# Optimization experiments

Hardware: AMD Instinct MI355X
Metric: run time of the kernel (lower is better)

## Reference

```python
import math
import jax, jax.numpy as jnp
import numpy as np

DIMS = 20
MULT = 8
K = (DIMS + 1) * MULT  # 168 mixture components
N = 524288
EPS = 1.0              # log_density default eps
BASE_COV = 0.1
LOG_NORM = -DIMS / 2 * math.log(2 * math.pi)


def setup_inputs() -> dict:
    key = jax.random.key(0)
    k1, k2, k3 = jax.random.split(key, 3)
    sample = jax.random.normal(k1, (N, DIMS), dtype=jnp.float32) * 0.3
    alpha = jax.random.normal(k2, (K,), dtype=jnp.float32) * 0.1
    mu = jax.random.uniform(k3, (K, DIMS), dtype=jnp.float32, minval=-0.5, maxval=0.5)
    cov = jnp.full((K, DIMS), BASE_COV, dtype=jnp.float32)
    return {"sample": sample, "alpha": alpha, "mu": mu, "cov": cov}


def reference(sample, alpha, mu, cov):
    # Faithful vectorization of the per-component Python loop in log_density.
    var = EPS ** 2
    weights = jax.nn.softmax(alpha)                       # [K]
    i = jnp.arange(K) // MULT                             # component group index, 0..DIMS
    d = jnp.arange(DIMS)
    # cov[:i] *= var  ->  scale first i dims of each component's cov by var
    scale = jnp.where(d[None, :] < i[:, None], var, 1.0)  # [K, D]
    inv = 1.0 / (cov * scale)                             # [K, D]
    # det_cov = var**i * (1/10)**(dims - i)  (exactly as in the source)
    fi = i.astype(jnp.float32)
    det_cov = var ** fi * BASE_COV ** (DIMS - fi)         # [K]
    sig_term = det_cov ** -0.5                            # [K]
    # quad[n,k] = sum_d (x[n,d]-mu[k,d])^2 * inv[k,d], expanded into GEMMs
    quad = (sample ** 2) @ inv.T \
           - 2.0 * (sample @ (mu * inv).T) \
           + jnp.sum(mu * mu * inv, axis=1)[None, :]      # [N, K]
    results = sig_term * jnp.exp(-0.5 * quad) * weights   # [N, K]
    density = results.sum(axis=1, keepdims=True)          # [N, 1]
    return jnp.log(density) + LOG_NORM
```

## Files before the change

kernel.cpp:

```cpp
#include <hip/hip_runtime.h>
#include <math.h>


#define DIMS     20
#define MULT     8
#define K_COMP   168
#define KC_PAD   176
#define BROW     72
#define BASE_COV 0.1f
#define LOG2E    1.4426950408889634f
#define LN2      0.6931471805599453f
#define LOG_NORM -18.378770664093453f
#define CPW      8
#define NB       1024

typedef _Float16 f16x8 __attribute__((ext_vector_type(8)));
typedef _Float16 f16x2 __attribute__((ext_vector_type(2)));
typedef float    f32x4 __attribute__((ext_vector_type(4)));
typedef unsigned int uint;
typedef uint u32x4 __attribute__((ext_vector_type(4)));

__device__ __forceinline__ uint pk(float lo, float hi) {
    return __builtin_bit_cast(uint, __builtin_amdgcn_cvt_pkrtz(lo, hi));
}
__device__ __forceinline__ uint pksq(uint a) {
    f16x2 v = __builtin_bit_cast(f16x2, a);
    return __builtin_bit_cast(uint, (f16x2)(v * v));
}

__global__ __launch_bounds__(256, 3) void gm_fused(const float* __restrict__ sample,
                                                   const float* __restrict__ alpha,
                                                   const float* __restrict__ mu,
                                                   const float* __restrict__ cov,
                                                   float* __restrict__ out) {
    __shared__ __attribute__((aligned(16))) _Float16 lds_T[KC_PAD][BROW];
    __shared__ float sh_logZ;
    const int tid = threadIdx.x;

    uint* bz = (uint*)&lds_T[0][0];
    for (int i = tid; i < KC_PAD * BROW / 2; i += 256) bz[i] = 0u;
    __syncthreads();

    if (tid < 64) {
        float a0 = (tid       < K_COMP) ? alpha[tid]       : -1e30f;
        float a1 = (tid + 64  < K_COMP) ? alpha[tid + 64]  : -1e30f;
        float a2 = (tid + 128 < K_COMP) ? alpha[tid + 128] : -1e30f;
        float m = fmaxf(fmaxf(a0, a1), a2);
        for (int msk = 32; msk; msk >>= 1) m = fmaxf(m, __shfl_xor(m, msk, 64));
        float s = __expf(a0 - m) + __expf(a1 - m) + __expf(a2 - m);
        for (int msk = 32; msk; msk >>= 1) s += __shfl_xor(s, msk, 64);
        if (tid == 0) sh_logZ = m + __logf(s);
    }
    __syncthreads();

    if (tid < K_COMP) {
        const int   n  = tid;
        const int   i  = n / MULT;
        const float fi = (float)i;
        const float var = 1.0f;
        float logdet = fi * __logf(var) + ((float)DIMS - fi) * __logf(BASE_COV);
        const float4* cvp = (const float4*)(cov + n * DIMS);
        const float4* mup = (const float4*)(mu + n * DIMS);
        float4 c0 = cvp[0], c1 = cvp[1], c2 = cvp[2], c3 = cvp[3], c4 = cvp[4];
        float4 m0 = mup[0], m1 = mup[1], m2 = mup[2], m3 = mup[3], m4 = mup[4];
        float C = 0.0f;
        auto emit = [&](int d, float cc, float mm) {
            float scale = (d < i) ? var : 1.0f;
            float inv   = 1.0f / (cc * scale);
            C += mm * mm * inv;
            lds_T[n][d]        = (_Float16)(-0.5f * inv * LOG2E);
            lds_T[n][DIMS + d] = (_Float16)(mm * inv * LOG2E);
        };
        emit( 0, c0.x, m0.x); emit( 1, c0.y, m0.y); emit( 2, c0.z, m0.z); emit( 3, c0.w, m0.w);
        emit( 4, c1.x, m1.x); emit( 5, c1.y, m1.y); emit( 6, c1.z, m1.z); emit( 7, c1.w, m1.w);
        emit( 8, c2.x, m2.x); emit( 9, c2.y, m2.y); emit(10, c2.z, m2.z); emit(11, c2.w, m2.w);
        emit(12, c3.x, m3.x); emit(13, c3.y, m3.y); emit(14, c3.z, m3.z); emit(15, c3.w, m3.w);
        emit(16, c4.x, m4.x); emit(17, c4.y, m4.y); emit(18, c4.z, m4.z); emit(19, c4.w, m4.w);
        float L2 = ((alpha[n] - sh_logZ) - 0.5f * logdet - 0.5f * C) * LOG2E;
        lds_T[n][2 * DIMS] = (_Float16)L2;
    } else if (tid < KC_PAD) {
        lds_T[tid][2 * DIMS] = (_Float16)(-65504.0f);
    }
    __syncthreads();

    const int w = tid >> 6, l = tid & 63, q = l >> 4, c = l & 15;
    const bool qa = (q & 1) != 0, qb = (q & 2) != 0;
    const uint onezero = 0x00003C00u;
    const f32x4 zero = { 0.f, 0.f, 0.f, 0.f };

#define LOAD_CF(T)                                                              \
    const f16x8 cf1_##T = *(const f16x8*)&lds_T[(T) * 16 + c][q * 8];           \
    const f16x8 cf2_##T = *(const f16x8*)&lds_T[(T) * 16 + c][32 + q * 8];
    LOAD_CF(0) LOAD_CF(1) LOAD_CF(2) LOAD_CF(3) LOAD_CF(4) LOAD_CF(5)
    LOAD_CF(6) LOAD_CF(7) LOAD_CF(8) LOAD_CF(9) LOAD_CF(10)
#undef LOAD_CF

    const int base = blockIdx.x * (64 * CPW) + w * 16;

#define DO_TILE(T)                                                              \
        {                                                                       \
            f32x4 acc = __builtin_amdgcn_mfma_f32_16x16x32_f16(cf1_##T, sf1, zero, 0, 0, 0); \
            acc       = __builtin_amdgcn_mfma_f32_16x16x32_f16(cf2_##T, sf2, acc,  0, 0, 0); \
            dens += (__builtin_amdgcn_exp2f(acc[0]) + __builtin_amdgcn_exp2f(acc[1]))        \
                  + (__builtin_amdgcn_exp2f(acc[2]) + __builtin_amdgcn_exp2f(acc[3]));       \
        }

#define DO_CHUNK(CC)                                                            \
    {                                                                           \
        const float4* rp = (const float4*)(sample + (size_t)(base + (CC) * 64 + c) * DIMS); \
        float4 r0 = rp[0], r1 = rp[1], r2 = rp[2], r3 = rp[3], r4 = rp[4];      \
        uint q0 = pk(r0.x, r0.y), q1 = pk(r0.z, r0.w);                          \
        uint q2 = pk(r1.x, r1.y), q3 = pk(r1.z, r1.w);                          \
        uint q4 = pk(r2.x, r2.y), q5 = pk(r2.z, r2.w);                          \
        uint q6 = pk(r3.x, r3.y), q7 = pk(r3.z, r3.w);                          \
        uint q8 = pk(r4.x, r4.y), q9 = pk(r4.z, r4.w);                          \
        uint s0 = pksq(q0), s1 = pksq(q1), s2 = pksq(q2), s3 = pksq(q3);        \
        uint s4 = pksq(q4), s5 = pksq(q5), s6 = pksq(q6), s7 = pksq(q7);        \
        uint s8 = pksq(q8), s9 = pksq(q9);                                      \
        uint f1_0 = qb ? (qa ? q2 : s8) : (qa ? s4 : s0);                       \
        uint f1_1 = qb ? (qa ? q3 : s9) : (qa ? s5 : s1);                       \
        uint f1_2 = qb ? (qa ? q4 : q0) : (qa ? s6 : s2);                       \
        uint f1_3 = qb ? (qa ? q5 : q1) : (qa ? s7 : s3);                       \
        uint f2_0 = qb ? 0u : (qa ? onezero : q6);                              \
        uint f2_1 = qb ? 0u : (qa ? 0u : q7);                                   \
        uint f2_2 = qb ? 0u : (qa ? 0u : q8);                                   \
        uint f2_3 = qb ? 0u : (qa ? 0u : q9);                                   \
        u32x4 w1 = { f1_0, f1_1, f1_2, f1_3 };                                  \
        u32x4 w2 = { f2_0, f2_1, f2_2, f2_3 };                                  \
        f16x8 sf1 = __builtin_bit_cast(f16x8, w1);                              \
        f16x8 sf2 = __builtin_bit_cast(f16x8, w2);                              \
        float dens = 0.0f;                                                      \
        DO_TILE(0) DO_TILE(1) DO_TILE(2) DO_TILE(3) DO_TILE(4) DO_TILE(5)       \
        DO_TILE(6) DO_TILE(7) DO_TILE(8) DO_TILE(9) DO_TILE(10)                 \
        dens += __shfl_xor(dens, 16, 64);                                       \
        dens += __shfl_xor(dens, 32, 64);                                       \
        if (l < 16)                                                             \
            out[base + (CC) * 64 + l] = LN2 * __builtin_amdgcn_logf(dens) + LOG_NORM; \
    }

    DO_CHUNK(0) DO_CHUNK(1) DO_CHUNK(2) DO_CHUNK(3)
    DO_CHUNK(4) DO_CHUNK(5) DO_CHUNK(6) DO_CHUNK(7)
#undef DO_CHUNK
#undef DO_TILE
}

extern "C" void kernel_launch(void* const* d_in, const int* in_sizes, int n_in,
                              void* d_out, int out_size, void* d_ws, size_t ws_size,
                              hipStream_t stream) {
    const float* sample = (const float*)d_in[0];
    const float* alpha  = (const float*)d_in[1];
    const float* mu     = (const float*)d_in[2];
    const float* cov    = (const float*)d_in[3];
    float* out = (float*)d_out;
    gm_fused<<<NB, 256, 0, stream>>>(sample, alpha, mu, cov, out);
}
```

Baseline: 96.06 us.

## Prefetch next chunk's sample rows and defer reductions to kernel end

Loads for the next chunk's sample rows are issued right after the current chunk is packed, so global memory latency overlaps with the MFMA and exp2 work. The single density accumulator is split into four independent partial sums to shorten the dependency chain. The cross-lane shuffle reductions, log and stores for all eight chunks are moved after the main loop, so those steps no longer sit between compute phases. This raises live register count (prefetch buffers and eight density values), which could affect occupancy at the launch bounds of 3 blocks per SIMD.

```diff
diff --git a/kernel.cpp b/kernel.cpp
--- a/kernel.cpp
+++ b/kernel.cpp
@@ -97,23 +97,33 @@
 
     const int base = blockIdx.x * (64 * CPW) + w * 16;
 
+    const float4* rp0 = (const float4*)(sample + (size_t)(base + c) * DIMS);
+    float4 r0 = rp0[0], r1 = rp0[1], r2 = rp0[2], r3 = rp0[3], r4 = rp0[4];
+
 #define DO_TILE(T)                                                              \
         {                                                                       \
             f32x4 acc = __builtin_amdgcn_mfma_f32_16x16x32_f16(cf1_##T, sf1, zero, 0, 0, 0); \
             acc       = __builtin_amdgcn_mfma_f32_16x16x32_f16(cf2_##T, sf2, acc,  0, 0, 0); \
-            dens += (__builtin_amdgcn_exp2f(acc[0]) + __builtin_amdgcn_exp2f(acc[1]))        \
-                  + (__builtin_amdgcn_exp2f(acc[2]) + __builtin_amdgcn_exp2f(acc[3]));       \
+            p0 += __builtin_amdgcn_exp2f(acc[0]);                               \
+            p1 += __builtin_amdgcn_exp2f(acc[1]);                               \
+            p2 += __builtin_amdgcn_exp2f(acc[2]);                               \
+            p3 += __builtin_amdgcn_exp2f(acc[3]);                               \
         }
 
 #define DO_CHUNK(CC)                                                            \
+    float dens_##CC;                                                            \
     {                                                                           \
-        const float4* rp = (const float4*)(sample + (size_t)(base + (CC) * 64 + c) * DIMS); \
-        float4 r0 = rp[0], r1 = rp[1], r2 = rp[2], r3 = rp[3], r4 = rp[4];      \
+                                      \
         uint q0 = pk(r0.x, r0.y), q1 = pk(r0.z, r0.w);                          \
         uint q2 = pk(r1.x, r1.y), q3 = pk(r1.z, r1.w);                          \
         uint q4 = pk(r2.x, r2.y), q5 = pk(r2.z, r2.w);                          \
         uint q6 = pk(r3.x, r3.y), q7 = pk(r3.z, r3.w);                          \
         uint q8 = pk(r4.x, r4.y), q9 = pk(r4.z, r4.w);                          \
+           \
+        if ((CC) + 1 < CPW) {                                                   \
+            const float4* np = (const float4*)(sample + (size_t)(base + ((CC) + 1) * 64 + c) * DIMS); \
+            r0 = np[0]; r1 = np[1]; r2 = np[2]; r3 = np[3]; r4 = np[4];         \
+        }                                                                       \
         uint s0 = pksq(q0), s1 = pksq(q1), s2 = pksq(q2), s3 = pksq(q3);        \
         uint s4 = pksq(q4), s5 = pksq(q5), s6 = pksq(q6), s7 = pksq(q7);        \
         uint s8 = pksq(q8), s9 = pksq(q9);                                      \
@@ -129,19 +139,27 @@
         u32x4 w2 = { f2_0, f2_1, f2_2, f2_3 };                                  \
         f16x8 sf1 = __builtin_bit_cast(f16x8, w1);                              \
         f16x8 sf2 = __builtin_bit_cast(f16x8, w2);                              \
-        float dens = 0.0f;                                                      \
+        float p0 = 0.f, p1 = 0.f, p2 = 0.f, p3 = 0.f;   \
         DO_TILE(0) DO_TILE(1) DO_TILE(2) DO_TILE(3) DO_TILE(4) DO_TILE(5)       \
         DO_TILE(6) DO_TILE(7) DO_TILE(8) DO_TILE(9) DO_TILE(10)                 \
-        dens += __shfl_xor(dens, 16, 64);                                       \
-        dens += __shfl_xor(dens, 32, 64);                                       \
-        if (l < 16)                                                             \
-            out[base + (CC) * 64 + l] = LN2 * __builtin_amdgcn_logf(dens) + LOG_NORM; \
+        dens_##CC = (p0 + p1) + (p2 + p3);                                      \
     }
 
     DO_CHUNK(0) DO_CHUNK(1) DO_CHUNK(2) DO_CHUNK(3)
     DO_CHUNK(4) DO_CHUNK(5) DO_CHUNK(6) DO_CHUNK(7)
 #undef DO_CHUNK
 #undef DO_TILE
+
+#define FINISH(CC)                                                              \
+    {                                                                           \
+        float dn = dens_##CC;                                                   \
+        dn += __shfl_xor(dn, 16, 64);                                           \
+        dn += __shfl_xor(dn, 32, 64);                                           \
+        if (l < 16) out[base + (CC) * 64 + l] = LN2 * __builtin_amdgcn_logf(dn) + LOG_NORM; \
+    }
+    FINISH(0) FINISH(1) FINISH(2) FINISH(3)
+    FINISH(4) FINISH(5) FINISH(6) FINISH(7)
+#undef FINISH
 }
 
 extern "C" void kernel_launch(void* const* d_in, const int* in_sizes, int n_in,
```

Result: slower. 213.6 us (+122.4%).
